# Kernel tuning notes

Hardware: AMD Instinct MI355X
Metric: run time of the kernel (lower is better)

Reference implementation:

```python
import jax, jax.numpy as jnp
import numpy as np
from jax import lax

# --- static config (mirrors DecodeDetectionsFast __init__) ---
CONF_THRESH = 0.01
IOU_THRESH = 0.45
TOP_K = 200
NMS_MAX = 400
IMG_H = 512.0
IMG_W = 512.0
NEG = -1e10  # sentinel for suppressed / invalid scores


def setup_inputs() -> dict:
    key = jax.random.key(0)
    # (batch, n_boxes, n_classes + 12); last 12 = [offsets(4), anchors(4), variances(4)]
    y_pred = jax.random.normal(key, (32, 24564, 93), dtype=jnp.float32)
    return {"y_pred": y_pred}


def _iou_one_vs_all(box, boxes):
    # box: (4,) [xmin,ymin,xmax,ymax]; boxes: (N,4). TF-style IoU (no area clamp,
    # intersection clamped at 0).
    ix1 = jnp.maximum(box[0], boxes[:, 0])
    iy1 = jnp.maximum(box[1], boxes[:, 1])
    ix2 = jnp.minimum(box[2], boxes[:, 2])
    iy2 = jnp.minimum(box[3], boxes[:, 3])
    inter = jnp.maximum(ix2 - ix1, 0.0) * jnp.maximum(iy2 - iy1, 0.0)
    area = (box[2] - box[0]) * (box[3] - box[1])
    areas = (boxes[:, 2] - boxes[:, 0]) * (boxes[:, 3] - boxes[:, 1])
    union = area + areas - inter
    return jnp.where(union > 0.0, inter / union, 0.0)


def _nms_topk_one(preds, scores):
    # preds: (N,6) rows [class_id, conf, xmin, ymin, xmax, ymax]; scores: (N,)
    boxes = preds[:, 2:6]

    def step(sc, _):
        i = jnp.argmax(sc)
        s = sc[i]
        sel_valid = s > NEG * 0.5
        iou = _iou_one_vs_all(boxes[i], boxes)
        sc_new = jnp.where(iou > IOU_THRESH, NEG, sc).at[i].set(NEG)
        sc_new = jnp.where(sel_valid, sc_new, sc)
        return sc_new, (i, sel_valid)

    _, (idxs, valid) = lax.scan(step, scores, None, length=NMS_MAX)
    cand = preds[idxs] * valid[:, None].astype(preds.dtype)  # (NMS_MAX, 6); invalid -> zero rows
    _, top_idx = lax.top_k(cand[:, 1], TOP_K)  # sort by confidence, zero-padded rows sink
    return cand[top_idx]


def reference(y_pred):
    n_classes = y_pred.shape[2] - 12
    cls_scores = y_pred[..., :n_classes]
    class_ids = jnp.argmax(cls_scores, axis=-1).astype(y_pred.dtype)  # (B,N)
    conf = jnp.max(cls_scores, axis=-1)  # (B,N)

    # decode centroid offsets with anchors and variances
    cx = y_pred[..., -12] * y_pred[..., -4] * y_pred[..., -6] + y_pred[..., -8]
    cy = y_pred[..., -11] * y_pred[..., -3] * y_pred[..., -5] + y_pred[..., -7]
    w = jnp.exp(y_pred[..., -10] * y_pred[..., -2]) * y_pred[..., -6]
    h = jnp.exp(y_pred[..., -9] * y_pred[..., -1]) * y_pred[..., -5]

    xmin = (cx - 0.5 * w) * IMG_W
    ymin = (cy - 0.5 * h) * IMG_H
    xmax = (cx + 0.5 * w) * IMG_W
    ymax = (cy + 0.5 * h) * IMG_H

    preds = jnp.stack([class_ids, conf, xmin, ymin, xmax, ymax], axis=-1)  # (B,N,6)

    # background (class 0) removal + confidence thresholding via score masking
    valid = (class_ids != 0.0) & (conf > CONF_THRESH)
    scores = jnp.where(valid, conf, NEG)

    return jax.vmap(_nms_topk_one)(preds, scores)  # (B, TOP_K, 6)
```

## Files before the change

### kernel.cpp

```cpp
#include <hip/hip_runtime.h>
#include <stdint.h>

#define NANCH 24564
#define NBATCH 32
#define NCLS 81
#define FEAT 93
#define NEGV -10000000000.0f
#define CONF_T 0.01f
#define IOU_T 0.45f
#define TOPK 200
#define CAP 1024
#define TARGET 768u
#define NBINS 1024
#define APB 64

__global__ __launch_bounds__(256) void decode_kernel(
    const float* __restrict__ yp, float4* __restrict__ boxes,
    float* __restrict__ scores, float* __restrict__ cls) {
#pragma clang fp contract(off)
  __shared__ float lds[APB * FEAT];
  const float4* src = (const float4*)yp + (size_t)blockIdx.x * (APB * FEAT / 4);
  float4* dst = (float4*)lds;
  for (int i = threadIdx.x; i < APB * FEAT / 4; i += 256) dst[i] = src[i];
  __syncthreads();
  int t = threadIdx.x;
  if (t < APB) {
    const float* p = &lds[t * FEAT];
    float best = -3.0e38f;
    int bi = 0;
    for (int c = 0; c < NCLS; ++c) {
      float v = p[c];
      if (v > best) { best = v; bi = c; }
    }
    float cx = p[81] * p[89] * p[87] + p[85];
    float cy = p[82] * p[90] * p[88] + p[86];
    float w  = expf(p[83] * p[91]) * p[87];
    float h  = expf(p[84] * p[92]) * p[88];
    float xmin = (cx - 0.5f * w) * 512.0f;
    float ymin = (cy - 0.5f * h) * 512.0f;
    float xmax = (cx + 0.5f * w) * 512.0f;
    float ymax = (cy + 0.5f * h) * 512.0f;
    int ga = blockIdx.x * APB + t;
    boxes[ga] = make_float4(xmin, ymin, xmax, ymax);
    cls[ga] = (float)bi;
    scores[ga] = (bi != 0 && best > CONF_T) ? best : NEGV;
  }
}

__device__ __forceinline__ bool iou_gt(float sx1, float sy1, float sx2, float sy2,
                                       float bx1, float by1, float bx2, float by2) {
#pragma clang fp contract(off)
  float ix1 = fmaxf(sx1, bx1);
  float iy1 = fmaxf(sy1, by1);
  float ix2 = fminf(sx2, bx2);
  float iy2 = fminf(sy2, by2);
  float inter = fmaxf(ix2 - ix1, 0.0f) * fmaxf(iy2 - iy1, 0.0f);
  float area_s = (sx2 - sx1) * (sy2 - sy1);
  float area_b = (bx2 - bx1) * (by2 - by1);
  float uni = area_s + area_b - inter;
  float iou = (uni > 0.0f) ? (inter / uni) : 0.0f;
  return iou > IOU_T;
}

__global__ __launch_bounds__(1024) void nms_kernel(
    const float4* __restrict__ boxes, const float* __restrict__ scores,
    const float* __restrict__ cls, float* __restrict__ out) {
#pragma clang fp contract(off)
  __shared__ unsigned long long keys[CAP];
  __shared__ float4 cbox[CAP];
  __shared__ unsigned int hist[NBINS];
  __shared__ float selb[TOPK * 5];
  __shared__ unsigned int sel_idx[TOPK];
  __shared__ float sel_score[TOPK];
  __shared__ unsigned int s_cnt;
  __shared__ int s_cutoff;
  __shared__ int s_nsel;

  const int b = blockIdx.x;
  const int tid = threadIdx.x;
  const size_t base = (size_t)b * NANCH;

  hist[tid] = 0u;
  if (tid == 0) { s_cnt = 0u; s_cutoff = 0; s_nsel = 0; }
  __syncthreads();
  for (int i = tid; i < NANCH; i += 1024) {
    float s = scores[base + i];
    if (s >= 0.0f) {
      int bin = (int)(s * ((float)NBINS / 6.0f));
      bin = bin > (NBINS - 1) ? (NBINS - 1) : bin;
      atomicAdd(&hist[bin], 1u);
    }
  }
  __syncthreads();

  for (int off = 1; off < NBINS; off <<= 1) {
    unsigned int tt = (tid + off < NBINS) ? hist[tid + off] : 0u;
    __syncthreads();
    hist[tid] += tt;
    __syncthreads();
  }
  {
    unsigned int sfx = hist[tid];
    unsigned int nxt = (tid < NBINS - 1) ? hist[tid + 1] : 0u;
    if (sfx >= TARGET && nxt < TARGET) s_cutoff = tid;
  }
  __syncthreads();
  float cutoffv = (float)s_cutoff * (6.0f / (float)NBINS);

  for (int i = tid; i < NANCH; i += 1024) {
    float s = scores[base + i];
    if (s >= cutoffv) {
      unsigned int pos = atomicAdd(&s_cnt, 1u);
      if (pos < CAP) {
        unsigned long long key =
            ((unsigned long long)__float_as_uint(s) << 32) |
            (unsigned long long)(~(unsigned int)i);
        keys[pos] = key;
      }
    }
  }
  __syncthreads();
  int cnt = (int)(s_cnt > CAP ? CAP : s_cnt);
  if (tid >= cnt) keys[tid] = 0ull;
  __syncthreads();

  for (int k = 2; k <= CAP; k <<= 1) {
    for (int j = k >> 1; j > 0; j >>= 1) {
      int i = tid;
      int ixj = i ^ j;
      if (ixj > i) {
        unsigned long long a = keys[i], c = keys[ixj];
        bool up = ((i & k) == 0);
        if (up ? (a < c) : (a > c)) { keys[i] = c; keys[ixj] = a; }
      }
      __syncthreads();
    }
  }

  {
    unsigned long long key = keys[tid];
    if (key != 0ull) {
      unsigned int idx = ~(unsigned int)(key & 0xFFFFFFFFull);
      cbox[tid] = boxes[base + idx];
    }
  }
  __syncthreads();

  if (tid < 64) {
    int lane = tid;
    float b0x=0,b0y=0,b0z=0,b0w=0, b1x=0,b1y=0,b1z=0,b1w=0;
    float b2x=0,b2y=0,b2z=0,b2w=0, b3x=0,b3y=0,b3z=0,b3w=0;
    unsigned int i0=0,i1=0,i2=0,i3=0;
    float s0=0,s1=0,s2=0,s3=0;
    int nsel = 0;
    unsigned long long nkey = keys[0];
    float4 nbox = cbox[0];
    for (int c = 0; c < cnt && nsel < TOPK; ++c) {
      unsigned long long key = nkey;
      float4 box = nbox;
      int cn = (c + 1 < cnt) ? c + 1 : c;
      nkey = keys[cn];
      nbox = cbox[cn];
      bool sup = false;
      if (lane < nsel)       sup |= iou_gt(b0x,b0y,b0z,b0w, box.x,box.y,box.z,box.w);
      if (64 + lane < nsel)  sup |= iou_gt(b1x,b1y,b1z,b1w, box.x,box.y,box.z,box.w);
      if (128 + lane < nsel) sup |= iou_gt(b2x,b2y,b2z,b2w, box.x,box.y,box.z,box.w);
      if (192 + lane < nsel) sup |= iou_gt(b3x,b3y,b3z,b3w, box.x,box.y,box.z,box.w);
      if (!__any(sup ? 1 : 0)) {
        if (lane == (nsel & 63)) {
          unsigned int idx = ~(unsigned int)(key & 0xFFFFFFFFull);
          float sc = __uint_as_float((unsigned int)(key >> 32));
          int slot = nsel >> 6;
          if (slot == 0)      { b0x=box.x; b0y=box.y; b0z=box.z; b0w=box.w; i0=idx; s0=sc; }
          else if (slot == 1) { b1x=box.x; b1y=box.y; b1z=box.z; b1w=box.w; i1=idx; s1=sc; }
          else if (slot == 2) { b2x=box.x; b2y=box.y; b2z=box.z; b2w=box.w; i2=idx; s2=sc; }
          else                { b3x=box.x; b3y=box.y; b3z=box.z; b3w=box.w; i3=idx; s3=sc; }
        }
        nsel++;
      }
    }
    if (lane < nsel)       { int r = lane;     selb[r*5+0]=b0x; selb[r*5+1]=b0y; selb[r*5+2]=b0z; selb[r*5+3]=b0w; sel_idx[r]=i0; sel_score[r]=s0; }
    if (64 + lane < nsel)  { int r = 64+lane;  selb[r*5+0]=b1x; selb[r*5+1]=b1y; selb[r*5+2]=b1z; selb[r*5+3]=b1w; sel_idx[r]=i1; sel_score[r]=s1; }
    if (128 + lane < nsel) { int r = 128+lane; selb[r*5+0]=b2x; selb[r*5+1]=b2y; selb[r*5+2]=b2z; selb[r*5+3]=b2w; sel_idx[r]=i2; sel_score[r]=s2; }
    if (192 + lane < nsel) { int r = 192+lane; selb[r*5+0]=b3x; selb[r*5+1]=b3y; selb[r*5+2]=b3z; selb[r*5+3]=b3w; sel_idx[r]=i3; sel_score[r]=s3; }
    if (lane == 0) s_nsel = nsel;
  }
  __syncthreads();

  int nsel = s_nsel;
  for (int e = tid; e < TOPK * 6; e += 1024) {
    int r = e / 6, col = e % 6;
    float v = 0.0f;
    if (r < nsel) {
      if (col == 0)      v = cls[base + sel_idx[r]];
      else if (col == 1) v = sel_score[r];
      else               v = selb[r * 5 + (col - 2)];
    }
    out[(size_t)b * (TOPK * 6) + e] = v;
  }
}

extern "C" void kernel_launch(void* const* d_in, const int* in_sizes, int n_in,
                              void* d_out, int out_size, void* d_ws, size_t ws_size,
                              hipStream_t stream) {
  const float* yp = (const float*)d_in[0];
  float* out = (float*)d_out;
  char* ws = (char*)d_ws;

  const int total_anch = NANCH * NBATCH;
  float4* boxes = (float4*)ws;
  float* scores = (float*)(ws + (size_t)total_anch * 16);
  float* cls    = (float*)(ws + (size_t)total_anch * 16 + (size_t)total_anch * 4);

  const int nblk = total_anch / APB;
  decode_kernel<<<nblk, 256, 0, stream>>>(yp, boxes, scores, cls);
  nms_kernel<<<NBATCH, 1024, 0, stream>>>(boxes, scores, cls, out);
}
```

Before: 501.5 us.

## Split class argmax across lanes, register-cache scores, use wave-shuffle scan and sort

The decode kernel now uses four lanes per anchor to find the class argmax and combines them with xor shuffles, so all 256 threads work instead of 64. The NMS kernel loads each thread's 24 scores into registers once, reusing them for the histogram and compaction passes instead of reading global memory twice. The suffix scan becomes a single-wave shuffle scan, and the bitonic sort does its stages with j below 64 via wave shuffles, keeping LDS and barriers only for the larger strides. This removes many __syncthreads and LDS round trips, at the cost of higher register pressure in a 1024-thread block.

Measured after the change: 489.9 us. 2.3% less time.

```diff
diff --git a/kernel.cpp b/kernel.cpp
--- a/kernel.cpp
+++ b/kernel.cpp
@@ -23,15 +23,27 @@
   float4* dst = (float4*)lds;
   for (int i = threadIdx.x; i < APB * FEAT / 4; i += 256) dst[i] = src[i];
   __syncthreads();
-  int t = threadIdx.x;
-  if (t < APB) {
-    const float* p = &lds[t * FEAT];
-    float best = -3.0e38f;
-    int bi = 0;
-    for (int c = 0; c < NCLS; ++c) {
-      float v = p[c];
-      if (v > best) { best = v; bi = c; }
-    }
+
+  const int L = threadIdx.x;
+  const int a = L >> 2;
+  const int part = L & 3;
+  const float* p = &lds[a * FEAT];
+
+  int c0 = part * 21;
+  int c1 = (part == 3) ? NCLS : c0 + 21;
+  float best = -3.0e38f;
+  int bi = c0;
+  for (int c = c0; c < c1; ++c) {
+    float v = p[c];
+    if (v > best) { best = v; bi = c; }
+  }
+  for (int off = 1; off < 4; off <<= 1) {
+    float ov = __shfl_xor(best, off, 64);
+    int   oi = __shfl_xor(bi, off, 64);
+    if (ov > best || (ov == best && oi < bi)) { best = ov; bi = oi; }
+  }
+
+  if (part == 0) {
     float cx = p[81] * p[89] * p[87] + p[85];
     float cy = p[82] * p[90] * p[88] + p[86];
     float w  = expf(p[83] * p[91]) * p[87];
@@ -40,7 +52,7 @@
     float ymin = (cy - 0.5f * h) * 512.0f;
     float xmax = (cx + 0.5f * w) * 512.0f;
     float ymax = (cy + 0.5f * h) * 512.0f;
-    int ga = blockIdx.x * APB + t;
+    int ga = blockIdx.x * APB + a;
     boxes[ga] = make_float4(xmin, ymin, xmax, ymax);
     cls[ga] = (float)bi;
     scores[ga] = (bi != 0 && best > CONF_T) ? best : NEGV;
@@ -62,6 +74,9 @@
   return iou > IOU_T;
 }
 
+__device__ __forceinline__ unsigned long long maxu64(unsigned long long a, unsigned long long b) { return a > b ? a : b; }
+__device__ __forceinline__ unsigned long long minu64(unsigned long long a, unsigned long long b) { return a < b ? a : b; }
+
 __global__ __launch_bounds__(1024) void nms_kernel(
     const float4* __restrict__ boxes, const float* __restrict__ scores,
     const float* __restrict__ cls, float* __restrict__ out) {
@@ -80,11 +95,19 @@
   const int tid = threadIdx.x;
   const size_t base = (size_t)b * NANCH;
 
+  float sreg[24];
+#pragma unroll
+  for (int j = 0; j < 24; ++j) {
+    int i = tid + j * 1024;
+    sreg[j] = (i < NANCH) ? scores[base + i] : NEGV;
+  }
+
   hist[tid] = 0u;
   if (tid == 0) { s_cnt = 0u; s_cutoff = 0; s_nsel = 0; }
   __syncthreads();
-  for (int i = tid; i < NANCH; i += 1024) {
-    float s = scores[base + i];
+#pragma unroll
+  for (int j = 0; j < 24; ++j) {
+    float s = sreg[j];
     if (s >= 0.0f) {
       int bin = (int)(s * ((float)NBINS / 6.0f));
       bin = bin > (NBINS - 1) ? (NBINS - 1) : bin;
@@ -93,12 +116,22 @@
   }
   __syncthreads();
 
-  for (int off = 1; off < NBINS; off <<= 1) {
-    unsigned int tt = (tid + off < NBINS) ? hist[tid + off] : 0u;
-    __syncthreads();
-    hist[tid] += tt;
-    __syncthreads();
-  }
+  if (tid < 64) {
+    int lane = tid;
+    unsigned int h[16];
+    unsigned int S = 0;
+#pragma unroll
+    for (int t = 0; t < 16; ++t) { h[t] = hist[lane * 16 + t]; S += h[t]; }
+    unsigned int incl = S;
+    for (int off = 1; off < 64; off <<= 1) {
+      unsigned int o = __shfl_down(incl, off, 64);
+      if (lane + off < 64) incl += o;
+    }
+    unsigned int acc = incl - S;
+#pragma unroll
+    for (int t = 15; t >= 0; --t) { acc += h[t]; hist[lane * 16 + t] = acc; }
+  }
+  __syncthreads();
   {
     unsigned int sfx = hist[tid];
     unsigned int nxt = (tid < NBINS - 1) ? hist[tid + 1] : 0u;
@@ -107,42 +140,50 @@
   __syncthreads();
   float cutoffv = (float)s_cutoff * (6.0f / (float)NBINS);
 
-  for (int i = tid; i < NANCH; i += 1024) {
-    float s = scores[base + i];
+#pragma unroll
+  for (int j = 0; j < 24; ++j) {
+    float s = sreg[j];
     if (s >= cutoffv) {
       unsigned int pos = atomicAdd(&s_cnt, 1u);
       if (pos < CAP) {
-        unsigned long long key =
-            ((unsigned long long)__float_as_uint(s) << 32) |
-            (unsigned long long)(~(unsigned int)i);
-        keys[pos] = key;
+        unsigned int i = (unsigned int)(tid + j * 1024);
+        keys[pos] = ((unsigned long long)__float_as_uint(s) << 32) |
+                    (unsigned long long)(~i);
       }
     }
   }
   __syncthreads();
   int cnt = (int)(s_cnt > CAP ? CAP : s_cnt);
-  if (tid >= cnt) keys[tid] = 0ull;
-  __syncthreads();
-
-  for (int k = 2; k <= CAP; k <<= 1) {
-    for (int j = k >> 1; j > 0; j >>= 1) {
-      int i = tid;
-      int ixj = i ^ j;
-      if (ixj > i) {
-        unsigned long long a = keys[i], c = keys[ixj];
-        bool up = ((i & k) == 0);
-        if (up ? (a < c) : (a > c)) { keys[i] = c; keys[ixj] = a; }
-      }
+
+  unsigned long long v = (tid < cnt) ? keys[tid] : 0ull;
+  for (int k = 2; k <= 64; k <<= 1) {
+    for (int j = k >> 1; j >= 1; j >>= 1) {
+      unsigned long long o = __shfl_xor((long long)v, j, 64);
+      bool keepmax = (((tid & k) == 0) == ((tid & j) == 0));
+      v = keepmax ? maxu64(v, o) : minu64(v, o);
+    }
+  }
+  for (int k = 128; k <= CAP; k <<= 1) {
+    for (int j = k >> 1; j >= 64; j >>= 1) {
+      keys[tid] = v;
       __syncthreads();
-    }
-  }
-
-  {
-    unsigned long long key = keys[tid];
-    if (key != 0ull) {
-      unsigned int idx = ~(unsigned int)(key & 0xFFFFFFFFull);
-      cbox[tid] = boxes[base + idx];
-    }
+      unsigned long long o = keys[tid ^ j];
+      bool keepmax = (((tid & k) == 0) == ((tid & j) == 0));
+      v = keepmax ? maxu64(v, o) : minu64(v, o);
+      __syncthreads();
+    }
+    for (int j = 32; j >= 1; j >>= 1) {
+      unsigned long long o = __shfl_xor((long long)v, j, 64);
+      bool keepmax = (((tid & k) == 0) == ((tid & j) == 0));
+      v = keepmax ? maxu64(v, o) : minu64(v, o);
+    }
+  }
+  keys[tid] = v;
+  __syncthreads();
+
+  if (v != 0ull) {
+    unsigned int idx = ~(unsigned int)(v & 0xFFFFFFFFull);
+    cbox[tid] = boxes[base + idx];
   }
   __syncthreads();
 
@@ -190,13 +231,13 @@
   int nsel = s_nsel;
   for (int e = tid; e < TOPK * 6; e += 1024) {
     int r = e / 6, col = e % 6;
-    float v = 0.0f;
+    float val = 0.0f;
     if (r < nsel) {
-      if (col == 0)      v = cls[base + sel_idx[r]];
-      else if (col == 1) v = sel_score[r];
-      else               v = selb[r * 5 + (col - 2)];
-    }
-    out[(size_t)b * (TOPK * 6) + e] = v;
+      if (col == 0)      val = cls[base + sel_idx[r]];
+      else if (col == 1) val = sel_score[r];
+      else               val = selb[r * 5 + (col - 2)];
+    }
+    out[(size_t)b * (TOPK * 6) + e] = val;
   }
 }
 
```
